# Kernel optimization log

Hardware: AMD Instinct MI355X
Metric: run time of the kernel (lower is better)

The kernel has to match this reference:

```python
import jax, jax.numpy as jnp
import numpy as np

N, W, MAX_DEPTH = 250_000, 784, 16
N_NODES = 2 ** MAX_DEPTH + 1  # 65537
DEPTH = MAX_DEPTH - 1  # deepest traversal that keeps indices in-range


def setup_inputs() -> dict:
    key = jax.random.key(0)
    k1, k2, k3 = jax.random.split(key, 3)
    x = jax.random.randint(k1, (N, W), 0, 2, dtype=jnp.int32)  # binary features
    node_choices = jax.random.randint(k2, (N_NODES,), 0, W, dtype=jnp.int32)
    node_predictions = jax.random.randint(k3, (N_NODES,), 0, 2).astype(jnp.float32)
    return {"x": x, "node_choices": node_choices,
            "node_predictions": node_predictions, "depth": DEPTH}


def reference(x, node_choices, node_predictions, depth):
    # Sequential decision-tree traversal: at each level gather the split
    # feature index for every sample's current node, read that feature bit,
    # and descend to child 2*n+1 (bit=0) or 2*n+2 (bit=1).
    n = x.shape[0]
    nodes0 = jnp.zeros((n,), dtype=jnp.int32)

    def body(_, nodes):
        choices = node_choices[nodes]                                   # [n]
        decisions = jnp.take_along_axis(x, choices[:, None].astype(jnp.int32), axis=1)[:, 0]
        return nodes * 2 + decisions + 1

    nodes = jax.lax.fori_loop(0, depth, body, nodes0)
    return node_predictions[nodes].astype(jnp.bool_)
```

## Files before the change

kernel.cpp:

```cpp
#include <hip/hip_runtime.h>
#include <hip/hip_bf16.h>

__global__ __launch_bounds__(256) void Tree_17867063951635_kernel(
    const int* __restrict__ x,
    const int* __restrict__ choices,
    const float* __restrict__ preds,
    const int* __restrict__ depth_p,
    int* __restrict__ out,
    int n, int w)
{
    const int i = blockIdx.x * blockDim.x + threadIdx.x;
    if (i >= n) return;

    const int depth = *depth_p;
    const int* __restrict__ row = x + (long long)i * (long long)w;

    int node = 0;
    for (int d = 0; d < depth; ++d) {
        const int c   = choices[node];
        const int bit = row[c];
        node = node * 2 + bit + 1;
    }
    out[i] = (preds[node] != 0.0f) ? 1 : 0;
}

extern "C" void kernel_launch(void* const* d_in, const int* in_sizes, int n_in,
                              void* d_out, int out_size, void* d_ws, size_t ws_size,
                              hipStream_t stream) {
    const int*   x       = (const int*)d_in[0];
    const int*   choices = (const int*)d_in[1];
    const float* preds   = (const float*)d_in[2];
    const int*   depth_p = (const int*)d_in[3];
    int*         out     = (int*)d_out;

    const int n = out_size;
    const int w = in_sizes[0] / n;

    const int block = 256;
    const int grid  = (n + block - 1) / block;
    Tree_17867063951635_kernel<<<grid, block, 0, stream>>>(
        x, choices, preds, depth_p, out, n, w);
}
```

Baseline: 913.0 us.

## Bit-pack feature rows in a prepass and traverse from LDS-staged bitmaps

Adds a pre-kernel that reads each 784-int row with coalesced wave loads and packs the bits into 13 uint64 words via ballot, written to workspace. The traversal kernel then stages 256 packed rows per block into LDS with vectorized loads and does the 15 lookups as bit extractions. The aim is to replace scattered, uncoalesced 4-byte gathers per level with one streaming read of x. The cost is a second launch, a full coalesced read of the ~784 MB input, and about 33 KB of LDS per block. Width is hardcoded to 784.

```diff
diff --git a/kernel.cpp b/kernel.cpp
--- a/kernel.cpp
+++ b/kernel.cpp
@@ -1,24 +1,73 @@
 #include <hip/hip_runtime.h>
 #include <hip/hip_bf16.h>
 
-__global__ __launch_bounds__(256) void Tree_17867063951635_kernel(
+
+#define W_FEAT    784
+#define NW64      13
+#define ROW_U64   16
+#define LDS_STRIDE 33
+
+__global__ __launch_bounds__(256) void tree_pack_kernel(
     const int* __restrict__ x,
+    unsigned long long* __restrict__ packed,
+    int n)
+{
+    const int row_i = (blockIdx.x * blockDim.x + threadIdx.x) >> 6;
+    const int lane  = threadIdx.x & 63;
+    if (row_i >= n) return;
+
+    const int* __restrict__ row = x + (long long)row_i * W_FEAT;
+    unsigned long long* __restrict__ orow = packed + (long long)row_i * ROW_U64;
+
+    unsigned long long myv = 0;
+    #pragma unroll
+    for (int k = 0; k < NW64; ++k) {
+        const int idx = k * 64 + lane;
+        int v = 0;
+        if (idx < W_FEAT) v = row[idx];
+        const unsigned long long b = __ballot(v & 1);
+        if (lane == k) myv = b;
+    }
+    if (lane < NW64) orow[lane] = myv;
+}
+
+__global__ __launch_bounds__(256) void tree_traverse_kernel(
+    const unsigned long long* __restrict__ packed,
     const int* __restrict__ choices,
     const float* __restrict__ preds,
     const int* __restrict__ depth_p,
     int* __restrict__ out,
-    int n, int w)
+    int n)
 {
-    const int i = blockIdx.x * blockDim.x + threadIdx.x;
+    __shared__ unsigned int lds[256 * LDS_STRIDE];
+
+    const int tid  = threadIdx.x;
+    const int base = blockIdx.x * 256;
+
+    const uint4* __restrict__ gp = (const uint4*)packed;
+    #pragma unroll
+    for (int it = 0; it < 8; ++it) {
+        const int idx = it * 256 + tid;
+        const int r   = idx >> 3;
+        const int c4  = idx & 7;
+        if (base + r < n) {
+            const uint4 v = gp[(long long)(base + r) * 8 + c4];
+            unsigned int* dst = &lds[r * LDS_STRIDE + c4 * 4];
+            dst[0] = v.x; dst[1] = v.y; dst[2] = v.z; dst[3] = v.w;
+        }
+    }
+    __syncthreads();
+
+    const int i = base + tid;
     if (i >= n) return;
 
     const int depth = *depth_p;
-    const int* __restrict__ row = x + (long long)i * (long long)w;
+    const unsigned int* __restrict__ row = &lds[tid * LDS_STRIDE];
 
     int node = 0;
     for (int d = 0; d < depth; ++d) {
         const int c   = choices[node];
-        const int bit = row[c];
+        const int bit = (row[c >> 5] >> (c & 31)) & 1;
         node = node * 2 + bit + 1;
     }
     out[i] = (preds[node] != 0.0f) ? 1 : 0;
@@ -34,10 +83,12 @@
     int*         out     = (int*)d_out;
 
     const int n = out_size;
-    const int w = in_sizes[0] / n;
+    unsigned long long* packed = (unsigned long long*)d_ws;
 
-    const int block = 256;
-    const int grid  = (n + block - 1) / block;
-    Tree_17867063951635_kernel<<<grid, block, 0, stream>>>(
-        x, choices, preds, depth_p, out, n, w);
+    const int pack_blocks = (n + 3) / 4;
+    tree_pack_kernel<<<pack_blocks, 256, 0, stream>>>(x, packed, n);
+
+    const int trav_blocks = (n + 255) / 256;
+    tree_traverse_kernel<<<trav_blocks, 256, 0, stream>>>(
+        packed, choices, preds, depth_p, out, n);
 }
```

Result: slower. 990.5 us (+8.5%).

## Stage rows as packed bitmasks in LDS via coalesced loads and ballot

Applied to the files above, without the earlier changes.

Each wave now streams 64 full rows of x with coalesced loads, packs each row's 784 binary features into 32-bit words with wave ballots, and stores them in shared memory. The traversal then reads the split bit from LDS instead of gathering scattered ints from global memory. This replaces 15 uncoalesced, latency-bound gathers per sample with one sequential pass over the whole input. In exchange it reads every feature rather than only the 15 visited ones. It also hardcodes the feature width of 784.

```diff
diff --git a/kernel.cpp b/kernel.cpp
--- a/kernel.cpp
+++ b/kernel.cpp
@@ -1,24 +1,61 @@
 #include <hip/hip_runtime.h>
 #include <hip/hip_bf16.h>
 
-__global__ __launch_bounds__(256) void Tree_17867063951635_kernel(
+
+#define W_FEAT 784
+#define NW64   13
+#define LSTR   27
+
+__global__ __launch_bounds__(256) void tree_fused_kernel(
     const int* __restrict__ x,
     const int* __restrict__ choices,
     const float* __restrict__ preds,
     const int* __restrict__ depth_p,
     int* __restrict__ out,
-    int n, int w)
+    int n)
 {
-    const int i = blockIdx.x * blockDim.x + threadIdx.x;
+    __shared__ unsigned int lds[256 * LSTR];
+
+    const int tid  = threadIdx.x;
+    const int wave = tid >> 6;
+    const int lane = tid & 63;
+    const int base = blockIdx.x * 256;
+
+    const int rbase = base + wave * 64;
+    for (int r = 0; r < 64; ++r) {
+        const int g = rbase + r;
+        if (g >= n) break;
+        const int* __restrict__ row = x + (long long)g * W_FEAT;
+
+        int v[NW64];
+        #pragma unroll
+        for (int k = 0; k < NW64; ++k) {
+            const int idx = k * 64 + lane;
+            v[k] = (idx < W_FEAT) ? row[idx] : 0;
+        }
+
+        unsigned int* __restrict__ dst = &lds[(wave * 64 + r) * LSTR];
+        #pragma unroll
+        for (int k = 0; k < NW64; ++k) {
+            const unsigned long long b = __ballot(v[k] & 1);
+            if (lane == k) {
+                dst[2 * k]     = (unsigned int)(b);
+                dst[2 * k + 1] = (unsigned int)(b >> 32);
+            }
+        }
+    }
+    __syncthreads();
+
+    const int i = base + tid;
     if (i >= n) return;
 
     const int depth = *depth_p;
-    const int* __restrict__ row = x + (long long)i * (long long)w;
+    const unsigned int* __restrict__ row = &lds[tid * LSTR];
 
     int node = 0;
     for (int d = 0; d < depth; ++d) {
         const int c   = choices[node];
-        const int bit = row[c];
+        const int bit = (row[c >> 5] >> (c & 31)) & 1;
         node = node * 2 + bit + 1;
     }
     out[i] = (preds[node] != 0.0f) ? 1 : 0;
@@ -34,10 +71,7 @@
     int*         out     = (int*)d_out;
 
     const int n = out_size;
-    const int w = in_sizes[0] / n;
-
-    const int block = 256;
-    const int grid  = (n + block - 1) / block;
-    Tree_17867063951635_kernel<<<grid, block, 0, stream>>>(
-        x, choices, preds, depth_p, out, n, w);
+    const int blocks = (n + 255) / 256;
+    tree_fused_kernel<<<blocks, 256, 0, stream>>>(
+        x, choices, preds, depth_p, out, n);
 }
```

Result: slower. 975.8 us (+6.9%).
